# Kernel tuning notes

Measured on AMD Instinct MI355X. Metric: run time of the kernel, lower is better.

## Reference

```python
import jax, jax.numpy as jnp
import numpy as np

F, H1, H2, K, L = 16, 64, 64, 8, 8          # n_features, hidden sizes, num_bins, num_layers
NBP = 3 * K + 1                              # num_bijector_params per feature
RMIN, RMAX = -10.0, 10.0
MIN_BIN, MIN_SLOPE = 1e-4, 1e-4              # distrax RationalQuadraticSpline defaults


def setup_inputs() -> dict:
    key = jax.random.key(0)
    ks = jax.random.split(key, 11)
    B = 131072
    return {
        "x": jax.random.normal(ks[0], (B, F), jnp.float32),
        "W0": jax.random.normal(ks[1], (L, F, F), jnp.float32) * 0.1,
        "b0": jax.random.normal(ks[2], (L, F), jnp.float32) * 0.01,
        "W1": jax.random.normal(ks[3], (L, F, H1), jnp.float32) * 0.1,
        "b1": jax.random.normal(ks[4], (L, H1), jnp.float32) * 0.01,
        "W2": jax.random.normal(ks[5], (L, H1, H2), jnp.float32) * 0.1,
        "b2": jax.random.normal(ks[6], (L, H2), jnp.float32) * 0.01,
        "Wout": jax.random.normal(ks[7], (L, H2, F * NBP), jnp.float32) * 0.05,
        "bout": jax.random.normal(ks[8], (L, F * NBP), jnp.float32) * 0.01,
        # scalar-affine coupling params; scale kept positive (init is ones in the module)
        "scale": jnp.exp(0.05 * jax.random.normal(ks[9], (L, F), jnp.float32)),
        "shift": jax.random.normal(ks[10], (L, F), jnp.float32) * 0.1,
    }


def _rq_spline_fwd(params, x):
    """distrax.RationalQuadraticSpline forward_and_log_det (elementwise).
    params: (B, F, 3K+1), x: (B, F) -> (y, log_det) each (B, F)."""
    uw, uh, ud = params[..., :K], params[..., K:2 * K], params[..., 2 * K:]
    total = RMAX - RMIN
    w = jax.nn.softmax(uw, axis=-1) * (total - K * MIN_BIN) + MIN_BIN   # bin widths
    h = jax.nn.softmax(uh, axis=-1) * (total - K * MIN_BIN) + MIN_BIN   # bin heights
    offset = float(np.log(np.expm1(1.0 - MIN_SLOPE)))                   # softplus(0+offset)=1
    d = jax.nn.softplus(ud + offset) + MIN_SLOPE                        # knot slopes (B,F,K+1)
    zeros = jnp.zeros(w.shape[:-1] + (1,), w.dtype)
    xpos = RMIN + jnp.concatenate([zeros, jnp.cumsum(w, -1)], -1)       # knot x (B,F,K+1)
    ypos = RMIN + jnp.concatenate([zeros, jnp.cumsum(h, -1)], -1)       # knot y (B,F,K+1)
    # per-element bin search
    idx = jnp.clip(jnp.sum((x[..., None] >= xpos).astype(jnp.int32), -1) - 1, 0, K - 1)
    take = lambda a: jnp.take_along_axis(a, idx[..., None], axis=-1)[..., 0]
    xk, xk1 = take(xpos[..., :-1]), take(xpos[..., 1:])
    yk, yk1 = take(ypos[..., :-1]), take(ypos[..., 1:])
    dk, dk1 = take(d[..., :-1]), take(d[..., 1:])
    bw = xk1 - xk
    bh = yk1 - yk
    s = bh / bw                                                          # bin slope
    z = jnp.clip((x - xk) / bw, 0.0, 1.0)
    z1m = 1.0 - z
    den = s + (dk1 + dk - 2.0 * s) * z * z1m
    y = yk + bh * (s * z * z + dk * z * z1m) / den
    num_ld = dk1 * z * z + 2.0 * s * z * z1m + dk * z1m * z1m
    ld = 2.0 * jnp.log(s) + jnp.log(num_ld) - 2.0 * jnp.log(den)
    outside = (x <= RMIN) | (x >= RMAX)                                  # identity outside range
    return jnp.where(outside, x, y), jnp.where(outside, 0.0, ld)


def reference(x, W0, b0, W1, b1, W2, b2, Wout, bout, scale, shift):
    """log_prob of Transformed(base, Inverse(Chain(layers))) == base.log_prob(Chain.fwd(x)) + fwd logdet."""
    B = x.shape[0]
    feat = jnp.arange(F)
    z = x
    logdet = jnp.zeros((B,), x.dtype)
    # distrax.Chain applies the last-appended layer first -> iterate layers in reverse;
    # within layer i: spline coupling (appended second) then scalar-affine coupling.
    for i in reversed(range(L)):
        mask = ((feat + i) % 2).astype(bool)        # True = pass-through / conditioner input
        mz = jnp.where(mask, z, 0.0)
        hid = jnp.tanh(mz @ W0[i] + b0[i])
        hid = jnp.tanh(hid @ W1[i] + b1[i])
        hid = hid @ W2[i] + b2[i]                   # last MLP layer is linear
        p = (hid @ Wout[i] + bout[i]).reshape(B, F, NBP)
        y, ld = _rq_spline_fwd(p, z)
        z = jnp.where(mask, z, y)
        logdet = logdet + jnp.sum(jnp.where(mask, 0.0, ld), axis=-1)
        # scalar affine coupling with all-False mask: transforms every feature
        z = z * scale[i] + shift[i]
        logdet = logdet + jnp.sum(jnp.log(jnp.abs(scale[i])))
    base_lp = -0.5 * jnp.sum(z * z, axis=-1) - 0.5 * F * float(np.log(2.0 * np.pi))
    return base_lp + logdet
```

## Files before the change

### kernel.cpp

```cpp
#include <hip/hip_runtime.h>
#include <math.h>

typedef _Float16 f16;
typedef _Float16 half8 __attribute__((ext_vector_type(8)));
typedef float f32x16 __attribute__((ext_vector_type(16)));

#define DEV __device__ __forceinline__

#define W1F_OFF 0
#define W2F_OFF 16384
#define WOF_OFF 81920
#define BOF_OFF 344064
#define SUMLOG_OFF 352256

#define WCHUNK    6400
#define H_STRIDE  144
#define P_SLOT    3200
#define P_STRIDE  100
#define LDS_BYTES 25600

DEV float frcp(float x){ return __builtin_amdgcn_rcpf(x); }
DEV float fexp(float x){ return __expf(x); }
DEV float flog(float x){ return __logf(x); }

DEV float ftanh(float x){
  float e = fexp(2.f * x);
  float r = frcp(e + 1.f);
  return fmaf(-2.f, r, 1.f);
}

DEV void rq_spline(const float p[25], float xv, float &y_out, float &ld_out)
{
  float ew[8]; float sw = 0.f;
#pragma unroll
  for (int k = 0; k < 8; ++k){ ew[k] = fexp(p[k]); sw += ew[k]; }
  float rw = frcp(sw) * 19.9992f;

  float xpos[9];
  xpos[0] = -10.f;
#pragma unroll
  for (int k = 0; k < 8; ++k) xpos[k + 1] = xpos[k] + fmaf(ew[k], rw, 1e-4f);

  int idx = 0;
#pragma unroll
  for (int j = 1; j < 8; ++j) idx += (xv >= xpos[j]) ? 1 : 0;

  float xk = xpos[0], ewk = ew[0];
#pragma unroll
  for (int j = 1; j < 8; ++j){
    bool sel = (idx >= j);
    xk  = sel ? xpos[j] : xk;
    ewk = sel ? ew[j]   : ewk;
  }
  float bw = fmaf(ewk, rw, 1e-4f);

  float eh[8]; float shs = 0.f;
#pragma unroll
  for (int k = 0; k < 8; ++k){ eh[k] = fexp(p[8 + k]); shs += eh[k]; }
  float rh = frcp(shs) * 19.9992f;

  float S = 0.f, ehk = eh[0];
#pragma unroll
  for (int k = 1; k < 8; ++k){
    bool sel = (idx >= k);
    S   += sel ? eh[k - 1] : 0.f;
    ehk  = sel ? eh[k]     : ehk;
  }
  float yk = fmaf(S, rh, fmaf((float)idx, 1e-4f, -10.f));
  float bh = fmaf(ehk, rh, 1e-4f);

  float uA = p[16], uB = p[17];
#pragma unroll
  for (int j = 1; j < 8; ++j){
    bool sel = (idx >= j);
    uA = sel ? p[16 + j] : uA;
    uB = sel ? p[17 + j] : uB;
  }
  float vA = uA + 0.54116666f;
  float dk  = fmaxf(vA, 0.f) + flog(1.f + fexp(-fabsf(vA))) + 1e-4f;
  float vB = uB + 0.54116666f;
  float dk1 = fmaxf(vB, 0.f) + flog(1.f + fexp(-fabsf(vB))) + 1e-4f;

  float rbw = frcp(bw);
  float s   = bh * rbw;
  float zf  = fminf(fmaxf((xv - xk) * rbw, 0.f), 1.f);
  float z1  = 1.f - zf;
  float zz  = zf * zf, z01 = zf * z1;
  float den = s + (dk1 + dk - 2.f * s) * z01;
  float rden = frcp(den);
  float yv  = yk + bh * (s * zz + dk * z01) * rden;
  float num = dk1 * zz + 2.f * s * z01 + dk * z1 * z1;
  float ldv = flog(s * s * num * rden * rden);

  bool outside = (xv <= -10.f) || (xv >= 10.f);
  y_out  = outside ? xv : yv;
  ld_out = outside ? 0.f : ldv;
}

extern "C" __global__ void __launch_bounds__(256)
prep_kernel(const float* __restrict__ W1, const float* __restrict__ W2,
            const float* __restrict__ Wo, const float* __restrict__ bout,
            const float* __restrict__ scale, char* __restrict__ ws)
{
  int tid = blockIdx.x * 256 + threadIdx.x;
  if (tid < 1024){
    int fi = tid >> 6, lane = tid & 63;
    int l = fi >> 1, nt = fi & 1;
    int n = nt * 32 + (lane & 31), khi = lane >> 5;
    half8 h;
#pragma unroll
    for (int j = 0; j < 8; ++j){ int k = khi * 8 + j; h[j] = (f16)W1[l * 1024 + k * 64 + n]; }
    *(half8*)(ws + W1F_OFF + fi * 1024 + lane * 16) = h;
  } else if (tid < 5120){
    int idx = tid - 1024;
    int fi = idx >> 6, lane = idx & 63;
    int l = fi >> 3, kt = (fi >> 1) & 3, nt = fi & 1;
    int n = nt * 32 + (lane & 31), khi = lane >> 5;
    half8 h;
#pragma unroll
    for (int j = 0; j < 8; ++j){ int k = kt * 16 + khi * 8 + j; h[j] = (f16)W2[l * 4096 + k * 64 + n]; }
    *(half8*)(ws + W2F_OFF + fi * 1024 + lane * 16) = h;
  } else if (tid < 21504){
    int idx = tid - 5120;
    int fi = idx >> 6, lane = idx & 63;
    int l = fi >> 5, u = (fi >> 2) & 7, kt = fi & 3;
    int f = (l & 1) + 2 * u;
    int c = lane & 31, khi = lane >> 5;
    half8 h;
#pragma unroll
    for (int j = 0; j < 8; ++j){
      int k = kt * 16 + khi * 8 + j;
      float v = (c < 25) ? Wo[l * 25600 + k * 400 + f * 25 + c] : 0.f;
      h[j] = (f16)v;
    }
    *(half8*)(ws + WOF_OFF + fi * 1024 + lane * 16) = h;
  } else if (tid < 23552){
    int idx = tid - 21504;
    int l = idx >> 8, u = (idx >> 5) & 7, c = idx & 31;
    int f = (l & 1) + 2 * u;
    float v = (c < 25) ? bout[l * 400 + f * 25 + c] : 0.f;
    ((float*)(ws + BOF_OFF))[idx] = v;
  } else if (tid == 23552){
    float acc = 0.f;
    for (int i = 0; i < 128; ++i) acc += logf(fabsf(scale[i]));
    *(float*)(ws + SUMLOG_OFF) = acc;
  }
}

template<int PAR>
DEV void layer_mfma(int l,
                    const float* __restrict__ W0, const float* __restrict__ b0,
                    const float* __restrict__ b1v, const float* __restrict__ b2v,
                    const float* __restrict__ scv, const float* __restrict__ shv,
                    const char* __restrict__ ws, char* wlds ,
                    float (&z)[16], float &logdet,
                    int lane, int ln31, int khi)
{
  const float* w0  = W0 + l * 256;
  const float* bb0 = b0 + l * 16;
  const int rowbase = khi * 4;

  const half8* W1F = (const half8*)(ws + W1F_OFF);
  const half8* W2F = (const half8*)(ws + W2F_OFF);
  half8 w1f[2];
#pragma unroll
  for (int nt = 0; nt < 2; ++nt) w1f[nt] = W1F[(l * 2 + nt) * 64 + lane];
  float bias1[2], bias2[2];
#pragma unroll
  for (int nt = 0; nt < 2; ++nt){
    bias1[nt] = b1v[l * 64 + nt * 32 + ln31];
    bias2[nt] = b2v[l * 64 + nt * 32 + ln31];
  }

  float h0[16];
#pragma unroll
  for (int j = 0; j < 16; ++j) h0[j] = bb0[j];
#pragma unroll
  for (int u = 0; u < 8; ++u){
    const int f = (1 - PAR) + 2 * u;
    const float v = z[f];
#pragma unroll
    for (int j = 0; j < 16; ++j) h0[j] = fmaf(v, w0[f * 16 + j], h0[j]);
  }
  half8 a0;
#pragma unroll
  for (int j = 0; j < 8; ++j){
    float hv = khi ? h0[j + 8] : h0[j];
    a0[j] = (f16)ftanh(hv);
  }

  f32x16 d1[2];
#pragma unroll
  for (int nt = 0; nt < 2; ++nt)
#pragma unroll
    for (int i = 0; i < 16; ++i) d1[nt][i] = bias1[nt];
#pragma unroll
  for (int nt = 0; nt < 2; ++nt)
    d1[nt] = __builtin_amdgcn_mfma_f32_32x32x16_f16(a0, w1f[nt], d1[nt], 0, 0, 0);

  half8 w2f[8];
#pragma unroll
  for (int kt = 0; kt < 4; ++kt)
#pragma unroll
    for (int nt = 0; nt < 2; ++nt)
      w2f[kt * 2 + nt] = W2F[((l * 4 + kt) * 2 + nt) * 64 + lane];

#pragma unroll
  for (int nt = 0; nt < 2; ++nt)
#pragma unroll
    for (int i = 0; i < 16; ++i){
      int row = (i & 3) + 8 * (i >> 2) + rowbase;
      *(f16*)(wlds + row * H_STRIDE + (nt * 32 + ln31) * 2) = (f16)ftanh(d1[nt][i]);
    }

  half8 a1[4];
#pragma unroll
  for (int kt = 0; kt < 4; ++kt)
    a1[kt] = *(const half8*)(wlds + ln31 * H_STRIDE + kt * 32 + khi * 16);
  f32x16 d2[2];
#pragma unroll
  for (int nt = 0; nt < 2; ++nt)
#pragma unroll
    for (int i = 0; i < 16; ++i) d2[nt][i] = bias2[nt];
#pragma unroll
  for (int kt = 0; kt < 4; ++kt)
#pragma unroll
    for (int nt = 0; nt < 2; ++nt)
      d2[nt] = __builtin_amdgcn_mfma_f32_32x32x16_f16(a1[kt], w2f[kt * 2 + nt], d2[nt], 0, 0, 0);
#pragma unroll
  for (int nt = 0; nt < 2; ++nt)
#pragma unroll
    for (int i = 0; i < 16; ++i){
      int row = (i & 3) + 8 * (i >> 2) + rowbase;
      *(f16*)(wlds + row * H_STRIDE + (nt * 32 + ln31) * 2) = (f16)d2[nt][i];
    }

  half8 a2[4];
#pragma unroll
  for (int kt = 0; kt < 4; ++kt)
    a2[kt] = *(const half8*)(wlds + ln31 * H_STRIDE + kt * 32 + khi * 16);

  const half8* WOF = (const half8*)(ws + WOF_OFF);
  const float* BOF = (const float*)(ws + BOF_OFF);
#pragma unroll 1
  for (int it = 0; it < 4; ++it){
    half8 bfA[4], bfB[4];
#pragma unroll
    for (int kt = 0; kt < 4; ++kt){
      bfA[kt] = WOF[((l * 8 + it) * 4 + kt) * 64 + lane];
      bfB[kt] = WOF[((l * 8 + it + 4) * 4 + kt) * 64 + lane];
    }
    float biasA = BOF[(l * 8 + it) * 32 + ln31];
    float biasB = BOF[(l * 8 + it + 4) * 32 + ln31];

    f32x16 dpA, dpB;
#pragma unroll
    for (int i = 0; i < 16; ++i){ dpA[i] = biasA; dpB[i] = biasB; }
#pragma unroll
    for (int kt = 0; kt < 4; ++kt){
      dpA = __builtin_amdgcn_mfma_f32_32x32x16_f16(a2[kt], bfA[kt], dpA, 0, 0, 0);
      dpB = __builtin_amdgcn_mfma_f32_32x32x16_f16(a2[kt], bfB[kt], dpB, 0, 0, 0);
    }
    if (ln31 < 25){
#pragma unroll
      for (int i = 0; i < 16; ++i){
        int row = (i & 3) + 8 * (i >> 2) + rowbase;
        *(float*)(wlds + row * P_STRIDE + ln31 * 4)          = dpA[i];
        *(float*)(wlds + P_SLOT + row * P_STRIDE + ln31 * 4) = dpB[i];
      }
    }
    const char* pb = wlds + khi * P_SLOT + ln31 * P_STRIDE;
    float p[25];
#pragma unroll
    for (int j = 0; j < 25; ++j) p[j] = *(const float*)(pb + j * 4);

    float xlo = z[PAR + 2 * it], xhi = z[PAR + 2 * it + 8];
    float xin = khi ? xhi : xlo;
    float y, ld;
    rq_spline(p, xin, y, ld);
    logdet += ld;
    z[PAR + 2 * it]     = khi ? xlo : y;
    z[PAR + 2 * it + 8] = khi ? y : xhi;
  }

#pragma unroll
  for (int it = 0; it < 4; ++it){
    float mine  = khi ? z[PAR + 2 * it + 8] : z[PAR + 2 * it];
    float other = __shfl_xor(mine, 32, 64);
    z[PAR + 2 * it]     = khi ? other : z[PAR + 2 * it];
    z[PAR + 2 * it + 8] = khi ? z[PAR + 2 * it + 8] : other;
  }

  const float* scp = scv + l * 16;
  const float* shp = shv + l * 16;
#pragma unroll
  for (int j = 0; j < 16; ++j)
    z[j] = fmaf(z[j], scp[j], shp[j]);
}

extern "C" __global__ void __launch_bounds__(256, 4)
flow_kernel(const float* __restrict__ x,
            const float* __restrict__ W0, const float* __restrict__ b0,
            const float* __restrict__ b1v, const float* __restrict__ b2v,
            const float* __restrict__ scv, const float* __restrict__ shv,
            const char* __restrict__ ws, float* __restrict__ out, int B)
{
  extern __shared__ char lds[];
  const int t    = threadIdx.x;
  const int lane = t & 63;
  const int wv   = t >> 6;
  const int ln31 = lane & 31;
  const int khi  = lane >> 5;
  char* wlds = lds + wv * WCHUNK;

  const int sid = wv * 32 + ln31;
  const int g   = blockIdx.x * 128 + sid;

  float z[16];
  const float4* xv = reinterpret_cast<const float4*>(x + (size_t)g * 16);
  float4 a0 = xv[0], a1 = xv[1], a2 = xv[2], a3 = xv[3];
  z[0]=a0.x; z[1]=a0.y; z[2]=a0.z; z[3]=a0.w;
  z[4]=a1.x; z[5]=a1.y; z[6]=a1.z; z[7]=a1.w;
  z[8]=a2.x; z[9]=a2.y; z[10]=a2.z; z[11]=a2.w;
  z[12]=a3.x; z[13]=a3.y; z[14]=a3.z; z[15]=a3.w;

  float logdet = 0.f;
  for (int l = 7; l >= 0; --l){
    if (l & 1) layer_mfma<1>(l, W0, b0, b1v, b2v, scv, shv, ws, wlds, z, logdet, lane, ln31, khi);
    else       layer_mfma<0>(l, W0, b0, b1v, b2v, scv, shv, ws, wlds, z, logdet, lane, ln31, khi);
  }

  float ldtot = logdet + __shfl_xor(logdet, 32, 64);

  float sumlog = *(const float*)(ws + SUMLOG_OFF);
  float ss = 0.f;
#pragma unroll
  for (int j = 0; j < 16; ++j) ss = fmaf(z[j], z[j], ss);
  if (khi == 0)
    out[g] = -0.5f * ss - 14.7030165f + ldtot + sumlog;
}

extern "C" void kernel_launch(void* const* d_in, const int* in_sizes, int n_in,
                              void* d_out, int out_size, void* d_ws, size_t ws_size,
                              hipStream_t stream)
{
  const float* x    = (const float*)d_in[0];
  const float* W0   = (const float*)d_in[1];
  const float* b0   = (const float*)d_in[2];
  const float* W1   = (const float*)d_in[3];
  const float* b1   = (const float*)d_in[4];
  const float* W2   = (const float*)d_in[5];
  const float* b2   = (const float*)d_in[6];
  const float* Wout = (const float*)d_in[7];
  const float* bout = (const float*)d_in[8];
  const float* scale= (const float*)d_in[9];
  const float* shift= (const float*)d_in[10];

  int B = in_sizes[0] / 16;

  hipLaunchKernelGGL(prep_kernel, dim3(93), dim3(256), 0, stream,
                     W1, W2, Wout, bout, scale, (char*)d_ws);

  hipLaunchKernelGGL(flow_kernel, dim3(B / 128), dim3(256), LDS_BYTES, stream,
                     x, W0, b0, b1, b2, scale, shift,
                     (const char*)d_ws, (float*)d_out, B);
}
```

Baseline: 216.4 us.

## Prefetch next output-weight tile, serialize MFMA accumulators, fuse spline bin search

The output-projection loop now prefetches the next iteration's A-half weight fragments and bias before the spline work, hiding global-load latency behind computation. The A and B MFMA chains are split into sequential scoped blocks, so only one 16-float accumulator is live at a time, which lowers register pressure. The spline bin search also drops the xpos array and instead computes the running cumulative knot position inside the selection loop. The trade-offs are extra live registers for the prefetched fragments and less MFMA interleaving between the two accumulators.

```diff
diff --git a/kernel.cpp b/kernel.cpp
--- a/kernel.cpp
+++ b/kernel.cpp
@@ -36,21 +36,16 @@
   for (int k = 0; k < 8; ++k){ ew[k] = fexp(p[k]); sw += ew[k]; }
   float rw = frcp(sw) * 19.9992f;
 
-  float xpos[9];
-  xpos[0] = -10.f;
-#pragma unroll
-  for (int k = 0; k < 8; ++k) xpos[k + 1] = xpos[k] + fmaf(ew[k], rw, 1e-4f);
-
   int idx = 0;
-#pragma unroll
-  for (int j = 1; j < 8; ++j) idx += (xv >= xpos[j]) ? 1 : 0;
-
-  float xk = xpos[0], ewk = ew[0];
+  float xk = -10.f, ewk = ew[0];
+  float cum = fmaf(ew[0], rw, -10.f + 1e-4f);
 #pragma unroll
   for (int j = 1; j < 8; ++j){
-    bool sel = (idx >= j);
-    xk  = sel ? xpos[j] : xk;
-    ewk = sel ? ew[j]   : ewk;
+    bool sel = (xv >= cum);
+    idx += sel ? 1 : 0;
+    xk  = sel ? cum   : xk;
+    ewk = sel ? ew[j] : ewk;
+    cum = fmaf(ew[j], rw, cum + 1e-4f);
   }
   float bw = fmaf(ewk, rw, 1e-4f);
 
@@ -162,6 +157,9 @@
 
   const half8* W1F = (const half8*)(ws + W1F_OFF);
   const half8* W2F = (const half8*)(ws + W2F_OFF);
+  const half8* WOF = (const half8*)(ws + WOF_OFF);
+  const float* BOF = (const float*)(ws + BOF_OFF);
+
   half8 w1f[2];
 #pragma unroll
   for (int nt = 0; nt < 2; ++nt) w1f[nt] = W1F[(l * 2 + nt) * 64 + lane];
@@ -227,6 +225,12 @@
 #pragma unroll
     for (int nt = 0; nt < 2; ++nt)
       d2[nt] = __builtin_amdgcn_mfma_f32_32x32x16_f16(a1[kt], w2f[kt * 2 + nt], d2[nt], 0, 0, 0);
+
+  half8 bfA[4];
+#pragma unroll
+  for (int kt = 0; kt < 4; ++kt) bfA[kt] = WOF[((l * 8 + 0) * 4 + kt) * 64 + lane];
+  float biasA = BOF[(l * 8 + 0) * 32 + ln31];
+
 #pragma unroll
   for (int nt = 0; nt < 2; ++nt)
 #pragma unroll
@@ -240,35 +244,50 @@
   for (int kt = 0; kt < 4; ++kt)
     a2[kt] = *(const half8*)(wlds + ln31 * H_STRIDE + kt * 32 + khi * 16);
 
-  const half8* WOF = (const half8*)(ws + WOF_OFF);
-  const float* BOF = (const float*)(ws + BOF_OFF);
 #pragma unroll 1
   for (int it = 0; it < 4; ++it){
-    half8 bfA[4], bfB[4];
-#pragma unroll
-    for (int kt = 0; kt < 4; ++kt){
-      bfA[kt] = WOF[((l * 8 + it) * 4 + kt) * 64 + lane];
-      bfB[kt] = WOF[((l * 8 + it + 4) * 4 + kt) * 64 + lane];
-    }
-    float biasA = BOF[(l * 8 + it) * 32 + ln31];
+    half8 bfB[4];
+#pragma unroll
+    for (int kt = 0; kt < 4; ++kt) bfB[kt] = WOF[((l * 8 + it + 4) * 4 + kt) * 64 + lane];
     float biasB = BOF[(l * 8 + it + 4) * 32 + ln31];
 
-    f32x16 dpA, dpB;
-#pragma unroll
-    for (int i = 0; i < 16; ++i){ dpA[i] = biasA; dpB[i] = biasB; }
-#pragma unroll
-    for (int kt = 0; kt < 4; ++kt){
-      dpA = __builtin_amdgcn_mfma_f32_32x32x16_f16(a2[kt], bfA[kt], dpA, 0, 0, 0);
-      dpB = __builtin_amdgcn_mfma_f32_32x32x16_f16(a2[kt], bfB[kt], dpB, 0, 0, 0);
-    }
-    if (ln31 < 25){
-#pragma unroll
-      for (int i = 0; i < 16; ++i){
-        int row = (i & 3) + 8 * (i >> 2) + rowbase;
-        *(float*)(wlds + row * P_STRIDE + ln31 * 4)          = dpA[i];
-        *(float*)(wlds + P_SLOT + row * P_STRIDE + ln31 * 4) = dpB[i];
+    {
+      f32x16 dp;
+#pragma unroll
+      for (int i = 0; i < 16; ++i) dp[i] = biasA;
+#pragma unroll
+      for (int kt = 0; kt < 4; ++kt)
+        dp = __builtin_amdgcn_mfma_f32_32x32x16_f16(a2[kt], bfA[kt], dp, 0, 0, 0);
+      if (ln31 < 25){
+#pragma unroll
+        for (int i = 0; i < 16; ++i){
+          int row = (i & 3) + 8 * (i >> 2) + rowbase;
+          *(float*)(wlds + row * P_STRIDE + ln31 * 4) = dp[i];
+        }
       }
     }
+    {
+      f32x16 dp;
+#pragma unroll
+      for (int i = 0; i < 16; ++i) dp[i] = biasB;
+#pragma unroll
+      for (int kt = 0; kt < 4; ++kt)
+        dp = __builtin_amdgcn_mfma_f32_32x32x16_f16(a2[kt], bfB[kt], dp, 0, 0, 0);
+      if (ln31 < 25){
+#pragma unroll
+        for (int i = 0; i < 16; ++i){
+          int row = (i & 3) + 8 * (i >> 2) + rowbase;
+          *(float*)(wlds + P_SLOT + row * P_STRIDE + ln31 * 4) = dp[i];
+        }
+      }
+    }
+
+    if (it < 3){
+#pragma unroll
+      for (int kt = 0; kt < 4; ++kt) bfA[kt] = WOF[((l * 8 + it + 1) * 4 + kt) * 64 + lane];
+      biasA = BOF[(l * 8 + it + 1) * 32 + ln31];
+    }
+
     const char* pb = wlds + khi * P_SLOT + ln31 * P_STRIDE;
     float p[25];
 #pragma unroll
```

Result: no change. 213.3 us (-1.4%).
